# Optimization experiments

Hardware: AMD Instinct MI355X
Metric: run time of the kernel (lower is better)

The kernel has to match this reference:

```python
import jax, jax.numpy as jnp
import numpy as np

N_LINKS = 262144
N_PAIRS = 4194304
F = 20   # feature_size
R = 20   # readout_units
T = 4    # message passing iterations


def setup_inputs() -> dict:
    key = jax.random.key(0)
    ks = jax.random.split(key, 16)
    s = 0.1
    return {
        "link_state": jax.random.normal(ks[0], (N_LINKS, F), dtype=jnp.float32),
        "first": jax.random.randint(ks[1], (N_PAIRS,), 0, N_LINKS),
        "second": jax.random.randint(ks[2], (N_PAIRS,), 0, N_LINKS),
        "state_dim": F,
        # message MLP: Linear(2F -> F)
        "W_msg": jax.random.normal(ks[3], (F, 2 * F), dtype=jnp.float32) * s,
        "b_msg": jnp.zeros((F,), dtype=jnp.float32),
        # GRUCell params (PyTorch layout: [3F, in] with r,z,n gate order)
        "W_ih": jax.random.normal(ks[4], (3 * F, F), dtype=jnp.float32) * s,
        "W_hh": jax.random.normal(ks[5], (3 * F, F), dtype=jnp.float32) * s,
        "b_ih": jnp.zeros((3 * F,), dtype=jnp.float32),
        "b_hh": jnp.zeros((3 * F,), dtype=jnp.float32),
        # readout: Linear(F->R) SELU, Linear(R->R) SELU
        "W_r1": jax.random.normal(ks[6], (R, F), dtype=jnp.float32) * s,
        "b_r1": jnp.zeros((R,), dtype=jnp.float32),
        "W_r2": jax.random.normal(ks[7], (R, R), dtype=jnp.float32) * s,
        "b_r2": jnp.zeros((R,), dtype=jnp.float32),
        # out layer: Linear(R->1)
        "W_out": jax.random.normal(ks[8], (1, R), dtype=jnp.float32) * s,
        "b_out": jnp.zeros((1,), dtype=jnp.float32),
    }


def _gru_cell(m, h, W_ih, W_hh, b_ih, b_hh):
    # PyTorch GRUCell math, gate order (r, z, n)
    gi = m @ W_ih.T + b_ih   # [N, 3F]
    gh = h @ W_hh.T + b_hh   # [N, 3F]
    i_r, i_z, i_n = jnp.split(gi, 3, axis=1)
    h_r, h_z, h_n = jnp.split(gh, 3, axis=1)
    r = jax.nn.sigmoid(i_r + h_r)
    z = jax.nn.sigmoid(i_z + h_z)
    n = jnp.tanh(i_n + r * h_n)
    return (1.0 - z) * n + z * h


def reference(link_state, first, second, state_dim,
              W_msg, b_msg, W_ih, W_hh, b_ih, b_hh,
              W_r1, b_r1, W_r2, b_r2, W_out, b_out):
    state = link_state  # [N_LINKS, F]
    for _ in range(T):
        main_edges = state[first]    # gather [N_PAIRS, F]
        neigh_edges = state[second]  # gather [N_PAIRS, F]
        edges_concat = jnp.concatenate([main_edges, neigh_edges], axis=1)
        m = jax.nn.selu(edges_concat @ W_msg.T + b_msg)  # [N_PAIRS, F]
        agg = jnp.zeros_like(state).at[second].add(m)    # scatter_add back to links
        state = _gru_cell(agg, state, W_ih, W_hh, b_ih, b_hh)
    feature = jnp.sum(state, axis=0)  # [F]
    h1 = jax.nn.selu(W_r1 @ feature + b_r1)
    h2 = jax.nn.selu(W_r2 @ h1 + b_r2)
    return W_out @ h2 + b_out  # [1]
```

## Files before the change

### kernel.cpp

```cpp
#include <hip/hip_runtime.h>
#include <hip/hip_fp16.h>

#define N_LINKS 262144
#define N_PAIRS 4194304
#define F 20
#define XB 20
#define T_ITERS 4

#define NSB 256
#define LPS 1024
#define PB 256
#define PT 1024
#define PCHUNK (N_PAIRS / PB)
#define PPT (PCHUNK / PT)

typedef float f32x2 __attribute__((ext_vector_type(2)));
typedef _Float16 h16x2 __attribute__((ext_vector_type(2)));

__device__ __forceinline__ float selu_f(float x) {
    const float scale = 1.0507009873554805f;
    const float scale_alpha = 1.7580993408473766f;
    return x > 0.0f ? scale * x : scale_alpha * (__expf(x) - 1.0f);
}

__device__ __forceinline__ float selu_b(float x) {
    const float s = 1.0507009873554805f;
    const float sa = 1.7580993408473766f;
    const float mx = fmaxf(x, 0.0f);
    const float mn = fminf(x, 0.0f);
    return fmaf(sa, __expf(mn), fmaf(s, mx, -sa));
}

__device__ __forceinline__ float sigmoid_f(float x) {
    return 1.0f / (1.0f + __expf(-x));
}

__device__ __forceinline__ float tanh_fast(float x) {
    x = fminf(fmaxf(x, -15.0f), 15.0f);
    float e = __expf(2.0f * x);
    return (e - 1.0f) / (e + 1.0f);
}

__device__ __forceinline__ void store_row_fp8(unsigned char* rowp, const float* o1) {
    int* p = (int*)rowp;
#pragma unroll
    for (int i = 0; i < 5; ++i) {
        int w = 0;
        w = __builtin_amdgcn_cvt_pk_fp8_f32(o1[4*i+0], o1[4*i+1], w, false);
        w = __builtin_amdgcn_cvt_pk_fp8_f32(o1[4*i+2], o1[4*i+3], w, true);
        p[i] = w;
    }
}


__global__ void __launch_bounds__(PT)
k_part(const int* __restrict__ first, const int* __restrict__ second,
       int* __restrict__ ent, int* __restrict__ ptable, int* __restrict__ sectot) {
    __shared__ int hist[NSB];
    __shared__ int cur[NSB];
    const int b = blockIdx.x;
    const int cbase = b * PCHUNK;
    const int tid = threadIdx.x;
    for (int i = tid; i < NSB; i += PT) hist[i] = 0;
    __syncthreads();
    int sv[PPT];
#pragma unroll
    for (int k = 0; k < PPT; ++k) {
        sv[k] = second[cbase + k * PT + tid];
        atomicAdd(&hist[sv[k] >> 10], 1);
    }
    __syncthreads();
    if (tid < NSB) {
        int acc = 0;
        for (int j = 0; j < tid; ++j) acc += hist[j];
        cur[tid] = acc;
        ptable[b * (NSB + 1) + tid] = acc;
        if (tid == 0) ptable[b * (NSB + 1) + NSB] = PCHUNK;
        atomicAdd(&sectot[tid], hist[tid]);
    }
    __syncthreads();
#pragma unroll
    for (int k = 0; k < PPT; ++k) {
        const int s = sv[k];
        const int f = first[cbase + k * PT + tid];
        const int pos = atomicAdd(&cur[s >> 10], 1);
        ent[cbase + pos] = f | ((s & 1023) << 18);
    }
}

__global__ void k_scan256(const int* __restrict__ sectot, int* __restrict__ sbase,
                          int* __restrict__ rs) {
    __shared__ int s[NSB];
    const int t = threadIdx.x;
    s[t] = sectot[t];
    __syncthreads();
    if (t == 0) {
        int acc = 0;
        for (int j = 0; j < NSB; ++j) { int c = s[j]; s[j] = acc; acc += c; }
    }
    __syncthreads();
    sbase[t] = s[t];
    if (t == 0) { sbase[NSB] = N_PAIRS; rs[N_LINKS] = N_PAIRS; }
}

__global__ void __launch_bounds__(PT)
k_build(const int* __restrict__ ptable, const int* __restrict__ sbase,
        const int* __restrict__ ent, int* __restrict__ srcs, int* __restrict__ rs,
        int* __restrict__ lid) {
    __shared__ int rstart[PB];
    __shared__ int rlen[PB];
    __shared__ int lcnt[LPS];
    __shared__ int cur[LPS];
    __shared__ int dhist[64];
    __shared__ int dbase[64];
    __shared__ int dcur[64];
    const int sb = blockIdx.x;
    const int tid = threadIdx.x;
    if (tid < PB) {
        const int o0 = ptable[tid * (NSB + 1) + sb];
        const int o1 = ptable[tid * (NSB + 1) + sb + 1];
        rstart[tid] = tid * PCHUNK + o0;
        rlen[tid] = o1 - o0;
    }
    lcnt[tid] = 0;
    if (tid < 64) { dhist[tid] = 0; dcur[tid] = 0; }
    __syncthreads();
    const int wave = tid >> 6;
    const int lane = tid & 63;
    for (int j = wave; j < PB; j += (PT >> 6)) {
        const int r0 = rstart[j], rl = rlen[j];
        for (int i = lane; i < rl; i += 64)
            atomicAdd(&lcnt[(ent[r0 + i] >> 18) & 1023], 1);
    }
    __syncthreads();
    const int count = lcnt[tid];
    const int dbin = min(count, 63);
    atomicAdd(&dhist[dbin], 1);
    __syncthreads();
    if (tid == 0) {
        int acc = 0;
        for (int b = 0; b < 64; ++b) { dbase[b] = acc; acc += dhist[b]; }
    }
    __syncthreads();
    const int rank = dbase[dbin] + atomicAdd(&dcur[dbin], 1);
    lcnt[rank] = count;
    lid[sb * LPS + rank] = sb * LPS + tid;
    __syncthreads();
    for (int off = 1; off < LPS; off <<= 1) {
        const int v = (tid >= off) ? lcnt[tid - off] : 0;
        __syncthreads();
        lcnt[tid] += v;
        __syncthreads();
    }
    const int sbb = sbase[sb];
    const int excl = lcnt[rank] - count;
    rs[sb * LPS + rank] = sbb + excl;
    cur[tid] = excl;
    __syncthreads();
    for (int j = wave; j < PB; j += (PT >> 6)) {
        const int r0 = rstart[j], rl = rlen[j];
        for (int i = lane; i < rl; i += 64) {
            const int e = ent[r0 + i];
            const int pos = atomicAdd(&cur[(e >> 18) & 1023], 1);
            srcs[sbb + pos] = e & 0x3FFFF;
        }
    }
}

__global__ void k_inv(const int* __restrict__ lid, int* __restrict__ rnk) {
    const int i = blockIdx.x * blockDim.x + threadIdx.x;
    rnk[lid[i]] = i;
}

__global__ void k_remap(int* __restrict__ srcs, const int* __restrict__ rnk) {
    const int p = blockIdx.x * blockDim.x + threadIdx.x;
    srcs[p] = rnk[srcs[p]] * 20;
}


__global__ void k_premsg(const float* __restrict__ link_state,
                         const int* __restrict__ lid,
                         const float* __restrict__ W_msg,
                         const float* __restrict__ b_msg,
                         unsigned char* __restrict__ X1b, __half* __restrict__ X2h,
                         float* __restrict__ state_r) {
    __shared__ float Wl[F * 2 * F];
    __shared__ float bl[F];
    for (int i = threadIdx.x; i < F * 2 * F; i += blockDim.x) Wl[i] = W_msg[i];
    if (threadIdx.x < F) bl[threadIdx.x] = b_msg[threadIdx.x];
    __syncthreads();

    const int slot = blockIdx.x * blockDim.x + threadIdx.x;
    const int link = lid[slot];

    float s[F];
    const float4* sp = (const float4*)(link_state + (size_t)link * F);
    float4* so = (float4*)(state_r + (size_t)slot * F);
#pragma unroll
    for (int i = 0; i < 5; ++i) {
        float4 v = sp[i];
        so[i] = v;
        s[4*i+0] = v.x; s[4*i+1] = v.y; s[4*i+2] = v.z; s[4*i+3] = v.w;
    }
    float o1[F], o2[F];
#pragma unroll
    for (int o = 0; o < F; ++o) {
        float a1 = bl[o], a2 = 0.0f;
#pragma unroll
        for (int k = 0; k < F; ++k) {
            a1 = fmaf(Wl[o * 2 * F + k],     s[k], a1);
            a2 = fmaf(Wl[o * 2 * F + F + k], s[k], a2);
        }
        o1[o] = a1; o2[o] = a2;
    }
    store_row_fp8(X1b + (size_t)slot * XB, o1);
    __half2* xp = (__half2*)(X2h + (size_t)slot * F);
#pragma unroll
    for (int i = 0; i < 10; ++i)
        xp[i] = __halves2half2(__float2half(o2[2*i]), __float2half(o2[2*i+1]));
}

__global__ void __launch_bounds__(256)
k_agg(const int* __restrict__ rs, const int* __restrict__ srcs,
      const unsigned char* __restrict__ X1b, const __half* __restrict__ X2h,
      float* __restrict__ agg) {
    const int wave = threadIdx.x >> 6;
    const int lane = threadIdx.x & 63;
    const int g = lane / 10;
    const int j = lane - g * 10;
    const int gsel = (g < 6) ? g : 5;
    const int slot = (blockIdx.x * 4 + wave) * 6 + gsel;

    const bool active = (g < 6) && (slot < N_LINKS);
    const int sc = min(slot, N_LINKS - 1);
    const int row_start = rs[sc];
    const int cnt = active ? (rs[sc + 1] - row_start) : 0;
    const int cl = (cnt > 0) ? (cnt - 1) : 0;

    const __half2 hv = *(const __half2*)(X2h + (size_t)sc * F + 2 * j);
    const float x2a = __half2float(__low2half(hv));
    const float x2b = __half2float(__high2half(hv));

    int cmax = cnt;
#pragma unroll
    for (int off = 1; off < 64; off <<= 1)
        cmax = max(cmax, __shfl_xor(cmax, off, 64));

    float acc_a = 0.0f, acc_b = 0.0f;

    for (int base = 0; base < cmax; base += 10) {
        const int sv = srcs[row_start + min(base + j, cl)];
#pragma unroll
        for (int r = 0; r < 10; ++r) {
            const int src = __shfl(sv, gsel * 10 + r, 64);
            const unsigned v = *(const unsigned short*)(X1b + src + 2 * j);
            const f32x2 xx = __builtin_amdgcn_cvt_pk_f32_fp8((int)v, false);
            const bool ok = (base + r) < cnt;
            acc_a += ok ? selu_b(xx[0] + x2a) : 0.0f;
            acc_b += ok ? selu_b(xx[1] + x2b) : 0.0f;
        }
    }
    if (active) {
        float2 o; o.x = acc_a; o.y = acc_b;
        *(float2*)(agg + (size_t)slot * F + 2 * j) = o;
    }
}

__global__ void __launch_bounds__(256)
k_gru(const float* __restrict__ agg, const float* __restrict__ h_in,
      const float* __restrict__ W_ih, const float* __restrict__ W_hh,
      const float* __restrict__ b_ih, const float* __restrict__ b_hh,
      const float* __restrict__ W_msg, const float* __restrict__ b_msg,
      float* __restrict__ h_out, unsigned char* __restrict__ X1b,
      __half* __restrict__ X2h, float* __restrict__ feature, int flags) {
    __shared__ h16x2 WiH[3 * F * 10];
    __shared__ h16x2 WhH[3 * F * 10];
    __shared__ h16x2 WmH[F * 20];
    __shared__ float bi[3 * F];
    __shared__ float bh[3 * F];
    __shared__ float bm[F];
    __shared__ float red[4 * F];
    {
        _Float16* wi = (_Float16*)WiH;
        _Float16* wh = (_Float16*)WhH;
        for (int i = threadIdx.x; i < 3 * F * F; i += blockDim.x) {
            wi[i] = (_Float16)W_ih[i];
            wh[i] = (_Float16)W_hh[i];
        }
        _Float16* wm = (_Float16*)WmH;
        for (int i = threadIdx.x; i < F * 2 * F; i += blockDim.x)
            wm[i] = (_Float16)W_msg[i];
    }
    if (threadIdx.x < 3 * F) {
        bi[threadIdx.x] = b_ih[threadIdx.x];
        bh[threadIdx.x] = b_hh[threadIdx.x];
    }
    if (threadIdx.x < F) bm[threadIdx.x] = b_msg[threadIdx.x];
    __syncthreads();

    const int l = blockIdx.x * blockDim.x + threadIdx.x;

    float m[F], h[F];
    const float4* mp = (const float4*)(agg  + (size_t)l * F);
    const float4* hp = (const float4*)(h_in + (size_t)l * F);
#pragma unroll
    for (int i = 0; i < 5; ++i) {
        float4 vm = mp[i], vh = hp[i];
        m[4*i+0] = vm.x; m[4*i+1] = vm.y; m[4*i+2] = vm.z; m[4*i+3] = vm.w;
        h[4*i+0] = vh.x; h[4*i+1] = vh.y; h[4*i+2] = vh.z; h[4*i+3] = vh.w;
    }
    h16x2 mh[10], hh[10];
#pragma unroll
    for (int i = 0; i < 10; ++i) {
        mh[i][0] = (_Float16)m[2*i]; mh[i][1] = (_Float16)m[2*i+1];
        hh[i][0] = (_Float16)h[2*i]; hh[i][1] = (_Float16)h[2*i+1];
    }

    float hn[F];
#pragma unroll
    for (int j = 0; j < F; ++j) {
        float gri = 0.f, gzi = 0.f, gin = bi[2*F + j];
        float grh = 0.f, gzh = 0.f, ghn = bh[2*F + j];
#pragma unroll
        for (int k = 0; k < 10; ++k) {
            gri = __builtin_amdgcn_fdot2(WiH[(0*F + j) * 10 + k], mh[k], gri, false);
            gzi = __builtin_amdgcn_fdot2(WiH[(1*F + j) * 10 + k], mh[k], gzi, false);
            gin = __builtin_amdgcn_fdot2(WiH[(2*F + j) * 10 + k], mh[k], gin, false);
            grh = __builtin_amdgcn_fdot2(WhH[(0*F + j) * 10 + k], hh[k], grh, false);
            gzh = __builtin_amdgcn_fdot2(WhH[(1*F + j) * 10 + k], hh[k], gzh, false);
            ghn = __builtin_amdgcn_fdot2(WhH[(2*F + j) * 10 + k], hh[k], ghn, false);
        }
        float r = sigmoid_f(bi[j] + bh[j] + gri + grh);
        float z = sigmoid_f(bi[F + j] + bh[F + j] + gzi + gzh);
        float n = tanh_fast(gin + r * ghn);
        hn[j] = (1.0f - z) * n + z * h[j];
    }

    float4* op = (float4*)(h_out + (size_t)l * F);
#pragma unroll
    for (int i = 0; i < 5; ++i)
        op[i] = make_float4(hn[4*i], hn[4*i+1], hn[4*i+2], hn[4*i+3]);

    if (flags & 1) {
        h16x2 hnh[10];
#pragma unroll
        for (int i = 0; i < 10; ++i) {
            hnh[i][0] = (_Float16)hn[2*i]; hnh[i][1] = (_Float16)hn[2*i+1];
        }
        float o1[F], o2[F];
#pragma unroll
        for (int o = 0; o < F; ++o) {
            float a1 = bm[o], a2 = 0.0f;
#pragma unroll
            for (int k = 0; k < 10; ++k) {
                a1 = __builtin_amdgcn_fdot2(WmH[o * 20 + k],      hnh[k], a1, false);
                a2 = __builtin_amdgcn_fdot2(WmH[o * 20 + 10 + k], hnh[k], a2, false);
            }
            o1[o] = a1; o2[o] = a2;
        }
        store_row_fp8(X1b + (size_t)l * XB, o1);
        __half2* xp = (__half2*)(X2h + (size_t)l * F);
#pragma unroll
        for (int i = 0; i < 10; ++i)
            xp[i] = __halves2half2(__float2half(o2[2*i]), __float2half(o2[2*i+1]));
    }

    if (flags & 2) {
#pragma unroll
        for (int off = 1; off < 64; off <<= 1) {
#pragma unroll
            for (int j = 0; j < F; ++j) hn[j] += __shfl_xor(hn[j], off, 64);
        }
        const int lane = threadIdx.x & 63;
        const int wave = threadIdx.x >> 6;
        if (lane == 0) {
#pragma unroll
            for (int j = 0; j < F; ++j) red[wave * F + j] = hn[j];
        }
        __syncthreads();
        if (threadIdx.x < F) {
            float s = red[threadIdx.x] + red[F + threadIdx.x] +
                      red[2 * F + threadIdx.x] + red[3 * F + threadIdx.x];
            atomicAdd(&feature[threadIdx.x], s);
        }
    }
}

__global__ void k_readout(const float* __restrict__ feature,
                          const float* __restrict__ W_r1, const float* __restrict__ b_r1,
                          const float* __restrict__ W_r2, const float* __restrict__ b_r2,
                          const float* __restrict__ W_out, const float* __restrict__ b_out,
                          float* __restrict__ out) {
    if (threadIdx.x != 0 || blockIdx.x != 0) return;
    float fv[F], h1[F], h2[F];
#pragma unroll
    for (int i = 0; i < F; ++i) fv[i] = feature[i];
#pragma unroll
    for (int o = 0; o < F; ++o) {
        float a = b_r1[o];
#pragma unroll
        for (int k = 0; k < F; ++k) a = fmaf(W_r1[o * F + k], fv[k], a);
        h1[o] = selu_f(a);
    }
#pragma unroll
    for (int o = 0; o < F; ++o) {
        float a = b_r2[o];
#pragma unroll
        for (int k = 0; k < F; ++k) a = fmaf(W_r2[o * F + k], h1[k], a);
        h2[o] = selu_f(a);
    }
    float a = b_out[0];
#pragma unroll
    for (int k = 0; k < F; ++k) a = fmaf(W_out[k], h2[k], a);
    out[0] = a;
}

extern "C" void kernel_launch(void* const* d_in, const int* in_sizes, int n_in,
                              void* d_out, int out_size, void* d_ws, size_t ws_size,
                              hipStream_t stream) {
    const float* link_state = (const float*)d_in[0];
    const int*   first      = (const int*)  d_in[1];
    const int*   second     = (const int*)  d_in[2];
    const float* W_msg = (const float*)d_in[4];
    const float* b_msg = (const float*)d_in[5];
    const float* W_ih  = (const float*)d_in[6];
    const float* W_hh  = (const float*)d_in[7];
    const float* b_ih  = (const float*)d_in[8];
    const float* b_hh  = (const float*)d_in[9];
    const float* W_r1  = (const float*)d_in[10];
    const float* b_r1  = (const float*)d_in[11];
    const float* W_r2  = (const float*)d_in[12];
    const float* b_r2  = (const float*)d_in[13];
    const float* W_out = (const float*)d_in[14];
    const float* b_out = (const float*)d_in[15];
    float* out = (float*)d_out;

    const size_t NF = (size_t)N_LINKS * F;
    float* state   = (float*)d_ws;
    float* agg     = state + NF;
    unsigned char* X1b = (unsigned char*)(agg + NF);
    __half* X2h    = (__half*)(X1b + (size_t)N_LINKS * XB + 64);
    int*    srcs   = (int*)(X2h + NF);
    int*    rs     = srcs + N_PAIRS;
    int*    lid    = rs + N_LINKS + 1;
    int*    rnk    = lid + N_LINKS;
    float* feature = (float*)(rnk + N_LINKS);
    int* ptable    = (int*)(feature + 32);
    int* sectot    = ptable + PB * (NSB + 1);
    int* sbase     = sectot + NSB;
    int* ent       = (int*)agg;

    hipMemsetAsync(sectot, 0, NSB * sizeof(int), stream);
    hipMemsetAsync(feature, 0, F * sizeof(float), stream);

    k_part<<<PB, PT, 0, stream>>>(first, second, ent, ptable, sectot);
    k_scan256<<<1, NSB, 0, stream>>>(sectot, sbase, rs);
    k_build<<<NSB, PT, 0, stream>>>(ptable, sbase, ent, srcs, rs, lid);
    k_inv<<<N_LINKS / 256, 256, 0, stream>>>(lid, rnk);
    k_remap<<<N_PAIRS / 256, 256, 0, stream>>>(srcs, rnk);

    k_premsg<<<N_LINKS / 256, 256, 0, stream>>>(link_state, lid, W_msg, b_msg,
                                                X1b, X2h, state);
    const int aggBlocks = (N_LINKS + 23) / 24;
    for (int t = 0; t < T_ITERS; ++t) {
        int flags = (t < T_ITERS - 1 ? 1 : 0) | (t == T_ITERS - 1 ? 2 : 0);
        k_agg<<<aggBlocks, 256, 0, stream>>>(rs, srcs, X1b, X2h, agg);
        k_gru<<<N_LINKS / 256, 256, 0, stream>>>(agg, state, W_ih, W_hh, b_ih, b_hh,
                                                 W_msg, b_msg, state, X1b, X2h,
                                                 feature, flags);
    }
    k_readout<<<1, 64, 0, stream>>>(feature, W_r1, b_r1, W_r2, b_r2, W_out, b_out, out);
}
```

Before: 601.3 us.

## Fuse aggregation and GRU into one step kernel with double-buffered fp8 messages

Merges the per-iteration aggregation and GRU kernels into a single k_step kernel. The GRU and next-message projection are computed cooperatively by 10 lanes per link, using shuffles to share the aggregated message and hidden state, so the agg buffer round trip through global memory goes away. The fp8 X1 table is double-buffered because other links still read the current buffer while it would otherwise be overwritten. The rank inverse is now written inside k_build, which drops the k_inv launch. In exchange, every step block (about 11k of them) reloads and converts the weights into shared memory, and the GRU maths is spread across lanes with extra shuffles.

```diff
diff --git a/kernel.cpp b/kernel.cpp
--- a/kernel.cpp
+++ b/kernel.cpp
@@ -106,7 +106,7 @@
 __global__ void __launch_bounds__(PT)
 k_build(const int* __restrict__ ptable, const int* __restrict__ sbase,
         const int* __restrict__ ent, int* __restrict__ srcs, int* __restrict__ rs,
-        int* __restrict__ lid) {
+        int* __restrict__ lid, int* __restrict__ rnk_g) {
     __shared__ int rstart[PB];
     __shared__ int rlen[PB];
     __shared__ int lcnt[LPS];
@@ -145,6 +145,7 @@
     const int rank = dbase[dbin] + atomicAdd(&dcur[dbin], 1);
     lcnt[rank] = count;
     lid[sb * LPS + rank] = sb * LPS + tid;
+    rnk_g[sb * LPS + tid] = sb * LPS + rank;
     __syncthreads();
     for (int off = 1; off < LPS; off <<= 1) {
         const int v = (tid >= off) ? lcnt[tid - off] : 0;
@@ -165,11 +166,6 @@
             srcs[sbb + pos] = e & 0x3FFFF;
         }
     }
-}
-
-__global__ void k_inv(const int* __restrict__ lid, int* __restrict__ rnk) {
-    const int i = blockIdx.x * blockDim.x + threadIdx.x;
-    rnk[lid[i]] = i;
 }
 
 __global__ void k_remap(int* __restrict__ srcs, const int* __restrict__ rnk) {
@@ -221,18 +217,50 @@
 }
 
 __global__ void __launch_bounds__(256)
-k_agg(const int* __restrict__ rs, const int* __restrict__ srcs,
-      const unsigned char* __restrict__ X1b, const __half* __restrict__ X2h,
-      float* __restrict__ agg) {
+k_step(const int* __restrict__ rs, const int* __restrict__ srcs,
+       const unsigned char* __restrict__ X1cur, unsigned char* __restrict__ X1nxt,
+       __half* __restrict__ X2h, float* __restrict__ state,
+       const float* __restrict__ W_ih, const float* __restrict__ W_hh,
+       const float* __restrict__ b_ih, const float* __restrict__ b_hh,
+       const float* __restrict__ W_msg, const float* __restrict__ b_msg,
+       float* __restrict__ feature, int flags) {
+    __shared__ h16x2 WiH[3 * F * 10];
+    __shared__ h16x2 WhH[3 * F * 10];
+    __shared__ h16x2 WmH[F * 20];
+    __shared__ float bi[3 * F];
+    __shared__ float bh[3 * F];
+    __shared__ float bm[F];
+    __shared__ float red[F];
+    {
+        _Float16* wi = (_Float16*)WiH;
+        _Float16* wh = (_Float16*)WhH;
+        for (int i = threadIdx.x; i < 3 * F * F; i += 256) {
+            wi[i] = (_Float16)W_ih[i];
+            wh[i] = (_Float16)W_hh[i];
+        }
+        _Float16* wm = (_Float16*)WmH;
+        for (int i = threadIdx.x; i < F * 2 * F; i += 256)
+            wm[i] = (_Float16)W_msg[i];
+    }
+    if (threadIdx.x < 3 * F) {
+        bi[threadIdx.x] = b_ih[threadIdx.x];
+        bh[threadIdx.x] = b_hh[threadIdx.x];
+    }
+    if (threadIdx.x < F) {
+        bm[threadIdx.x] = b_msg[threadIdx.x];
+        red[threadIdx.x] = 0.0f;
+    }
+    __syncthreads();
+
     const int wave = threadIdx.x >> 6;
     const int lane = threadIdx.x & 63;
     const int g = lane / 10;
     const int j = lane - g * 10;
     const int gsel = (g < 6) ? g : 5;
     const int slot = (blockIdx.x * 4 + wave) * 6 + gsel;
-
     const bool active = (g < 6) && (slot < N_LINKS);
     const int sc = min(slot, N_LINKS - 1);
+
     const int row_start = rs[sc];
     const int cnt = active ? (rs[sc + 1] - row_start) : 0;
     const int cl = (cnt > 0) ? (cnt - 1) : 0;
@@ -247,142 +275,93 @@
         cmax = max(cmax, __shfl_xor(cmax, off, 64));
 
     float acc_a = 0.0f, acc_b = 0.0f;
-
     for (int base = 0; base < cmax; base += 10) {
         const int sv = srcs[row_start + min(base + j, cl)];
 #pragma unroll
         for (int r = 0; r < 10; ++r) {
             const int src = __shfl(sv, gsel * 10 + r, 64);
-            const unsigned v = *(const unsigned short*)(X1b + src + 2 * j);
+            const unsigned v = *(const unsigned short*)(X1cur + src + 2 * j);
             const f32x2 xx = __builtin_amdgcn_cvt_pk_f32_fp8((int)v, false);
             const bool ok = (base + r) < cnt;
             acc_a += ok ? selu_b(xx[0] + x2a) : 0.0f;
             acc_b += ok ? selu_b(xx[1] + x2b) : 0.0f;
         }
     }
+
+    const float2 hown = *(const float2*)(state + (size_t)sc * F + 2 * j);
+    const int gb = gsel * 10;
+    h16x2 mh[10], hh[10];
+#pragma unroll
+    for (int kk = 0; kk < 10; ++kk) {
+        const float ma = __shfl(acc_a, gb + kk, 64);
+        const float mb = __shfl(acc_b, gb + kk, 64);
+        const float ha = __shfl(hown.x, gb + kk, 64);
+        const float hb = __shfl(hown.y, gb + kk, 64);
+        mh[kk][0] = (_Float16)ma; mh[kk][1] = (_Float16)mb;
+        hh[kk][0] = (_Float16)ha; hh[kk][1] = (_Float16)hb;
+    }
+
+    float hnv[2];
+    const float how[2] = {hown.x, hown.y};
+#pragma unroll
+    for (int t2 = 0; t2 < 2; ++t2) {
+        const int o = 2 * j + t2;
+        float gri = 0.f, gzi = 0.f, gin = bi[2*F + o];
+        float grh = 0.f, gzh = 0.f, ghn = bh[2*F + o];
+#pragma unroll
+        for (int kk = 0; kk < 10; ++kk) {
+            gri = __builtin_amdgcn_fdot2(WiH[(0*F + o) * 10 + kk], mh[kk], gri, false);
+            gzi = __builtin_amdgcn_fdot2(WiH[(1*F + o) * 10 + kk], mh[kk], gzi, false);
+            gin = __builtin_amdgcn_fdot2(WiH[(2*F + o) * 10 + kk], mh[kk], gin, false);
+            grh = __builtin_amdgcn_fdot2(WhH[(0*F + o) * 10 + kk], hh[kk], grh, false);
+            gzh = __builtin_amdgcn_fdot2(WhH[(1*F + o) * 10 + kk], hh[kk], gzh, false);
+            ghn = __builtin_amdgcn_fdot2(WhH[(2*F + o) * 10 + kk], hh[kk], ghn, false);
+        }
+        const float r = sigmoid_f(bi[o] + bh[o] + gri + grh);
+        const float z = sigmoid_f(bi[F + o] + bh[F + o] + gzi + gzh);
+        const float n = tanh_fast(gin + r * ghn);
+        hnv[t2] = (1.0f - z) * n + z * how[t2];
+    }
     if (active) {
-        float2 o; o.x = acc_a; o.y = acc_b;
-        *(float2*)(agg + (size_t)slot * F + 2 * j) = o;
-    }
-}
-
-__global__ void __launch_bounds__(256)
-k_gru(const float* __restrict__ agg, const float* __restrict__ h_in,
-      const float* __restrict__ W_ih, const float* __restrict__ W_hh,
-      const float* __restrict__ b_ih, const float* __restrict__ b_hh,
-      const float* __restrict__ W_msg, const float* __restrict__ b_msg,
-      float* __restrict__ h_out, unsigned char* __restrict__ X1b,
-      __half* __restrict__ X2h, float* __restrict__ feature, int flags) {
-    __shared__ h16x2 WiH[3 * F * 10];
-    __shared__ h16x2 WhH[3 * F * 10];
-    __shared__ h16x2 WmH[F * 20];
-    __shared__ float bi[3 * F];
-    __shared__ float bh[3 * F];
-    __shared__ float bm[F];
-    __shared__ float red[4 * F];
-    {
-        _Float16* wi = (_Float16*)WiH;
-        _Float16* wh = (_Float16*)WhH;
-        for (int i = threadIdx.x; i < 3 * F * F; i += blockDim.x) {
-            wi[i] = (_Float16)W_ih[i];
-            wh[i] = (_Float16)W_hh[i];
-        }
-        _Float16* wm = (_Float16*)WmH;
-        for (int i = threadIdx.x; i < F * 2 * F; i += blockDim.x)
-            wm[i] = (_Float16)W_msg[i];
-    }
-    if (threadIdx.x < 3 * F) {
-        bi[threadIdx.x] = b_ih[threadIdx.x];
-        bh[threadIdx.x] = b_hh[threadIdx.x];
-    }
-    if (threadIdx.x < F) bm[threadIdx.x] = b_msg[threadIdx.x];
-    __syncthreads();
-
-    const int l = blockIdx.x * blockDim.x + threadIdx.x;
-
-    float m[F], h[F];
-    const float4* mp = (const float4*)(agg  + (size_t)l * F);
-    const float4* hp = (const float4*)(h_in + (size_t)l * F);
-#pragma unroll
-    for (int i = 0; i < 5; ++i) {
-        float4 vm = mp[i], vh = hp[i];
-        m[4*i+0] = vm.x; m[4*i+1] = vm.y; m[4*i+2] = vm.z; m[4*i+3] = vm.w;
-        h[4*i+0] = vh.x; h[4*i+1] = vh.y; h[4*i+2] = vh.z; h[4*i+3] = vh.w;
-    }
-    h16x2 mh[10], hh[10];
-#pragma unroll
-    for (int i = 0; i < 10; ++i) {
-        mh[i][0] = (_Float16)m[2*i]; mh[i][1] = (_Float16)m[2*i+1];
-        hh[i][0] = (_Float16)h[2*i]; hh[i][1] = (_Float16)h[2*i+1];
-    }
-
-    float hn[F];
-#pragma unroll
-    for (int j = 0; j < F; ++j) {
-        float gri = 0.f, gzi = 0.f, gin = bi[2*F + j];
-        float grh = 0.f, gzh = 0.f, ghn = bh[2*F + j];
-#pragma unroll
-        for (int k = 0; k < 10; ++k) {
-            gri = __builtin_amdgcn_fdot2(WiH[(0*F + j) * 10 + k], mh[k], gri, false);
-            gzi = __builtin_amdgcn_fdot2(WiH[(1*F + j) * 10 + k], mh[k], gzi, false);
-            gin = __builtin_amdgcn_fdot2(WiH[(2*F + j) * 10 + k], mh[k], gin, false);
-            grh = __builtin_amdgcn_fdot2(WhH[(0*F + j) * 10 + k], hh[k], grh, false);
-            gzh = __builtin_amdgcn_fdot2(WhH[(1*F + j) * 10 + k], hh[k], gzh, false);
-            ghn = __builtin_amdgcn_fdot2(WhH[(2*F + j) * 10 + k], hh[k], ghn, false);
-        }
-        float r = sigmoid_f(bi[j] + bh[j] + gri + grh);
-        float z = sigmoid_f(bi[F + j] + bh[F + j] + gzi + gzh);
-        float n = tanh_fast(gin + r * ghn);
-        hn[j] = (1.0f - z) * n + z * h[j];
-    }
-
-    float4* op = (float4*)(h_out + (size_t)l * F);
-#pragma unroll
-    for (int i = 0; i < 5; ++i)
-        op[i] = make_float4(hn[4*i], hn[4*i+1], hn[4*i+2], hn[4*i+3]);
+        float2 o; o.x = hnv[0]; o.y = hnv[1];
+        *(float2*)(state + (size_t)slot * F + 2 * j) = o;
+    }
 
     if (flags & 1) {
         h16x2 hnh[10];
 #pragma unroll
-        for (int i = 0; i < 10; ++i) {
-            hnh[i][0] = (_Float16)hn[2*i]; hnh[i][1] = (_Float16)hn[2*i+1];
-        }
-        float o1[F], o2[F];
-#pragma unroll
-        for (int o = 0; o < F; ++o) {
+        for (int kk = 0; kk < 10; ++kk) {
+            const float na = __shfl(hnv[0], gb + kk, 64);
+            const float nb = __shfl(hnv[1], gb + kk, 64);
+            hnh[kk][0] = (_Float16)na; hnh[kk][1] = (_Float16)nb;
+        }
+        float o1v[2], o2v[2];
+#pragma unroll
+        for (int t2 = 0; t2 < 2; ++t2) {
+            const int o = 2 * j + t2;
             float a1 = bm[o], a2 = 0.0f;
 #pragma unroll
-            for (int k = 0; k < 10; ++k) {
-                a1 = __builtin_amdgcn_fdot2(WmH[o * 20 + k],      hnh[k], a1, false);
-                a2 = __builtin_amdgcn_fdot2(WmH[o * 20 + 10 + k], hnh[k], a2, false);
+            for (int kk = 0; kk < 10; ++kk) {
+                a1 = __builtin_amdgcn_fdot2(WmH[o * 20 + kk],      hnh[kk], a1, false);
+                a2 = __builtin_amdgcn_fdot2(WmH[o * 20 + 10 + kk], hnh[kk], a2, false);
             }
-            o1[o] = a1; o2[o] = a2;
-        }
-        store_row_fp8(X1b + (size_t)l * XB, o1);
-        __half2* xp = (__half2*)(X2h + (size_t)l * F);
-#pragma unroll
-        for (int i = 0; i < 10; ++i)
-            xp[i] = __halves2half2(__float2half(o2[2*i]), __float2half(o2[2*i+1]));
+            o1v[t2] = a1; o2v[t2] = a2;
+        }
+        if (active) {
+            const int w = __builtin_amdgcn_cvt_pk_fp8_f32(o1v[0], o1v[1], 0, false);
+            *(unsigned short*)(X1nxt + (size_t)slot * XB + 2 * j) = (unsigned short)w;
+            *(__half2*)(X2h + (size_t)slot * F + 2 * j) =
+                __halves2half2(__float2half(o2v[0]), __float2half(o2v[1]));
+        }
     }
 
     if (flags & 2) {
-#pragma unroll
-        for (int off = 1; off < 64; off <<= 1) {
-#pragma unroll
-            for (int j = 0; j < F; ++j) hn[j] += __shfl_xor(hn[j], off, 64);
-        }
-        const int lane = threadIdx.x & 63;
-        const int wave = threadIdx.x >> 6;
-        if (lane == 0) {
-#pragma unroll
-            for (int j = 0; j < F; ++j) red[wave * F + j] = hn[j];
+        if (active) {
+            atomicAdd(&red[2 * j],     hnv[0]);
+            atomicAdd(&red[2 * j + 1], hnv[1]);
         }
         __syncthreads();
-        if (threadIdx.x < F) {
-            float s = red[threadIdx.x] + red[F + threadIdx.x] +
-                      red[2 * F + threadIdx.x] + red[3 * F + threadIdx.x];
-            atomicAdd(&feature[threadIdx.x], s);
-        }
+        if (threadIdx.x < F) atomicAdd(&feature[threadIdx.x], red[threadIdx.x]);
     }
 }
 
@@ -436,38 +415,38 @@
     float* out = (float*)d_out;
 
     const size_t NF = (size_t)N_LINKS * F;
-    float* state   = (float*)d_ws;
-    float* agg     = state + NF;
-    unsigned char* X1b = (unsigned char*)(agg + NF);
-    __half* X2h    = (__half*)(X1b + (size_t)N_LINKS * XB + 64);
-    int*    srcs   = (int*)(X2h + NF);
-    int*    rs     = srcs + N_PAIRS;
-    int*    lid    = rs + N_LINKS + 1;
-    int*    rnk    = lid + N_LINKS;
+    float* state = (float*)d_ws;
+    unsigned char* X1b0 = (unsigned char*)(state + NF);
+    unsigned char* X1b1 = X1b0 + (size_t)N_LINKS * XB;
+    __half* X2h = (__half*)(X1b1 + (size_t)N_LINKS * XB);
+    int* srcs   = (int*)(X2h + NF);
+    int* rs     = srcs + N_PAIRS;
+    int* lid    = rs + N_LINKS + 1;
+    int* rnk    = lid + N_LINKS;
     float* feature = (float*)(rnk + N_LINKS);
-    int* ptable    = (int*)(feature + 32);
-    int* sectot    = ptable + PB * (NSB + 1);
-    int* sbase     = sectot + NSB;
-    int* ent       = (int*)agg;
+    int* ptable = (int*)(feature + 32);
+    int* sectot = ptable + PB * (NSB + 1);
+    int* sbase  = sectot + NSB;
+    int* ent    = (int*)X1b0;
 
     hipMemsetAsync(sectot, 0, NSB * sizeof(int), stream);
     hipMemsetAsync(feature, 0, F * sizeof(float), stream);
 
     k_part<<<PB, PT, 0, stream>>>(first, second, ent, ptable, sectot);
     k_scan256<<<1, NSB, 0, stream>>>(sectot, sbase, rs);
-    k_build<<<NSB, PT, 0, stream>>>(ptable, sbase, ent, srcs, rs, lid);
-    k_inv<<<N_LINKS / 256, 256, 0, stream>>>(lid, rnk);
+    k_build<<<NSB, PT, 0, stream>>>(ptable, sbase, ent, srcs, rs, lid, rnk);
     k_remap<<<N_PAIRS / 256, 256, 0, stream>>>(srcs, rnk);
 
     k_premsg<<<N_LINKS / 256, 256, 0, stream>>>(link_state, lid, W_msg, b_msg,
-                                                X1b, X2h, state);
-    const int aggBlocks = (N_LINKS + 23) / 24;
+                                                X1b0, X2h, state);
+
+    unsigned char* bufs[2] = {X1b0, X1b1};
+    const int stepBlocks = (N_LINKS + 23) / 24;
     for (int t = 0; t < T_ITERS; ++t) {
         int flags = (t < T_ITERS - 1 ? 1 : 0) | (t == T_ITERS - 1 ? 2 : 0);
-        k_agg<<<aggBlocks, 256, 0, stream>>>(rs, srcs, X1b, X2h, agg);
-        k_gru<<<N_LINKS / 256, 256, 0, stream>>>(agg, state, W_ih, W_hh, b_ih, b_hh,
-                                                 W_msg, b_msg, state, X1b, X2h,
-                                                 feature, flags);
+        k_step<<<stepBlocks, 256, 0, stream>>>(rs, srcs, bufs[t & 1], bufs[(t + 1) & 1],
+                                               X2h, state, W_ih, W_hh, b_ih, b_hh,
+                                               W_msg, b_msg, feature, flags);
     }
     k_readout<<<1, 64, 0, stream>>>(feature, W_r1, b_r1, W_r2, b_r2, W_out, b_out, out);
 }
```

Result: slower. 673.2 us (+12.0%).

## Process two links per GRU thread and fold rank inversion into build

Applied to the files above, without the earlier changes.

The GRU kernel now handles two links per thread. It loads each weight row from LDS into registers once and reuses it for both links, halving the grid size. The separate inverse-permutation kernel is removed, and k_build writes the rank table directly. This cuts LDS weight reads and one launch, but raises register pressure, which may reduce occupancy for the GRU kernel.

```diff
diff --git a/kernel.cpp b/kernel.cpp
--- a/kernel.cpp
+++ b/kernel.cpp
@@ -106,7 +106,7 @@
 __global__ void __launch_bounds__(PT)
 k_build(const int* __restrict__ ptable, const int* __restrict__ sbase,
         const int* __restrict__ ent, int* __restrict__ srcs, int* __restrict__ rs,
-        int* __restrict__ lid) {
+        int* __restrict__ lid, int* __restrict__ rnk_g) {
     __shared__ int rstart[PB];
     __shared__ int rlen[PB];
     __shared__ int lcnt[LPS];
@@ -145,6 +145,7 @@
     const int rank = dbase[dbin] + atomicAdd(&dcur[dbin], 1);
     lcnt[rank] = count;
     lid[sb * LPS + rank] = sb * LPS + tid;
+    rnk_g[sb * LPS + tid] = sb * LPS + rank;
     __syncthreads();
     for (int off = 1; off < LPS; off <<= 1) {
         const int v = (tid >= off) ? lcnt[tid - off] : 0;
@@ -165,11 +166,6 @@
             srcs[sbb + pos] = e & 0x3FFFF;
         }
     }
-}
-
-__global__ void k_inv(const int* __restrict__ lid, int* __restrict__ rnk) {
-    const int i = blockIdx.x * blockDim.x + threadIdx.x;
-    rnk[lid[i]] = i;
 }
 
 __global__ void k_remap(int* __restrict__ srcs, const int* __restrict__ rnk) {
@@ -267,12 +263,12 @@
 }
 
 __global__ void __launch_bounds__(256)
-k_gru(const float* __restrict__ agg, const float* __restrict__ h_in,
+k_gru(const float* __restrict__ agg, float* __restrict__ state,
       const float* __restrict__ W_ih, const float* __restrict__ W_hh,
       const float* __restrict__ b_ih, const float* __restrict__ b_hh,
       const float* __restrict__ W_msg, const float* __restrict__ b_msg,
-      float* __restrict__ h_out, unsigned char* __restrict__ X1b,
-      __half* __restrict__ X2h, float* __restrict__ feature, int flags) {
+      unsigned char* __restrict__ X1b, __half* __restrict__ X2h,
+      float* __restrict__ feature, int flags) {
     __shared__ h16x2 WiH[3 * F * 10];
     __shared__ h16x2 WhH[3 * F * 10];
     __shared__ h16x2 WmH[F * 20];
@@ -283,12 +279,12 @@
     {
         _Float16* wi = (_Float16*)WiH;
         _Float16* wh = (_Float16*)WhH;
-        for (int i = threadIdx.x; i < 3 * F * F; i += blockDim.x) {
+        for (int i = threadIdx.x; i < 3 * F * F; i += 256) {
             wi[i] = (_Float16)W_ih[i];
             wh[i] = (_Float16)W_hh[i];
         }
         _Float16* wm = (_Float16*)WmH;
-        for (int i = threadIdx.x; i < F * 2 * F; i += blockDim.x)
+        for (int i = threadIdx.x; i < F * 2 * F; i += 256)
             wm[i] = (_Float16)W_msg[i];
     }
     if (threadIdx.x < 3 * F) {
@@ -298,84 +294,146 @@
     if (threadIdx.x < F) bm[threadIdx.x] = b_msg[threadIdx.x];
     __syncthreads();
 
-    const int l = blockIdx.x * blockDim.x + threadIdx.x;
-
-    float m[F], h[F];
-    const float4* mp = (const float4*)(agg  + (size_t)l * F);
-    const float4* hp = (const float4*)(h_in + (size_t)l * F);
-#pragma unroll
-    for (int i = 0; i < 5; ++i) {
-        float4 vm = mp[i], vh = hp[i];
-        m[4*i+0] = vm.x; m[4*i+1] = vm.y; m[4*i+2] = vm.z; m[4*i+3] = vm.w;
-        h[4*i+0] = vh.x; h[4*i+1] = vh.y; h[4*i+2] = vh.z; h[4*i+3] = vh.w;
-    }
-    h16x2 mh[10], hh[10];
-#pragma unroll
-    for (int i = 0; i < 10; ++i) {
-        mh[i][0] = (_Float16)m[2*i]; mh[i][1] = (_Float16)m[2*i+1];
-        hh[i][0] = (_Float16)h[2*i]; hh[i][1] = (_Float16)h[2*i+1];
-    }
-
-    float hn[F];
-#pragma unroll
-    for (int j = 0; j < F; ++j) {
-        float gri = 0.f, gzi = 0.f, gin = bi[2*F + j];
-        float grh = 0.f, gzh = 0.f, ghn = bh[2*F + j];
-#pragma unroll
-        for (int k = 0; k < 10; ++k) {
-            gri = __builtin_amdgcn_fdot2(WiH[(0*F + j) * 10 + k], mh[k], gri, false);
-            gzi = __builtin_amdgcn_fdot2(WiH[(1*F + j) * 10 + k], mh[k], gzi, false);
-            gin = __builtin_amdgcn_fdot2(WiH[(2*F + j) * 10 + k], mh[k], gin, false);
-            grh = __builtin_amdgcn_fdot2(WhH[(0*F + j) * 10 + k], hh[k], grh, false);
-            gzh = __builtin_amdgcn_fdot2(WhH[(1*F + j) * 10 + k], hh[k], gzh, false);
-            ghn = __builtin_amdgcn_fdot2(WhH[(2*F + j) * 10 + k], hh[k], ghn, false);
-        }
-        float r = sigmoid_f(bi[j] + bh[j] + gri + grh);
-        float z = sigmoid_f(bi[F + j] + bh[F + j] + gzi + gzh);
-        float n = tanh_fast(gin + r * ghn);
-        hn[j] = (1.0f - z) * n + z * h[j];
-    }
-
-    float4* op = (float4*)(h_out + (size_t)l * F);
-#pragma unroll
-    for (int i = 0; i < 5; ++i)
-        op[i] = make_float4(hn[4*i], hn[4*i+1], hn[4*i+2], hn[4*i+3]);
+    const int l0 = (blockIdx.x * blockDim.x + threadIdx.x) * 2;
+
+    h16x2 mh[2][10], hh[2][10];
+#pragma unroll
+    for (int L = 0; L < 2; ++L) {
+        const float4* mp = (const float4*)(agg   + (size_t)(l0 + L) * F);
+        const float4* hp = (const float4*)(state + (size_t)(l0 + L) * F);
+#pragma unroll
+        for (int i = 0; i < 5; ++i) {
+            const float4 vm = mp[i], vh = hp[i];
+            mh[L][2*i+0][0] = (_Float16)vm.x; mh[L][2*i+0][1] = (_Float16)vm.y;
+            mh[L][2*i+1][0] = (_Float16)vm.z; mh[L][2*i+1][1] = (_Float16)vm.w;
+            hh[L][2*i+0][0] = (_Float16)vh.x; hh[L][2*i+0][1] = (_Float16)vh.y;
+            hh[L][2*i+1][0] = (_Float16)vh.z; hh[L][2*i+1][1] = (_Float16)vh.w;
+        }
+    }
+
+    float hn[2][F];
+#pragma unroll
+    for (int o = 0; o < F; ++o) {
+        float sr[2], sz[2], sni[2], snh[2];
+        {
+            h16x2 wi[10], wh[10];
+#pragma unroll
+            for (int kk = 0; kk < 10; ++kk) {
+                wi[kk] = WiH[(0*F + o) * 10 + kk];
+                wh[kk] = WhH[(0*F + o) * 10 + kk];
+            }
+#pragma unroll
+            for (int L = 0; L < 2; ++L) {
+                float a = bi[o] + bh[o];
+#pragma unroll
+                for (int kk = 0; kk < 10; ++kk) {
+                    a = __builtin_amdgcn_fdot2(wi[kk], mh[L][kk], a, false);
+                    a = __builtin_amdgcn_fdot2(wh[kk], hh[L][kk], a, false);
+                }
+                sr[L] = a;
+            }
+        }
+        {
+            h16x2 wi[10], wh[10];
+#pragma unroll
+            for (int kk = 0; kk < 10; ++kk) {
+                wi[kk] = WiH[(1*F + o) * 10 + kk];
+                wh[kk] = WhH[(1*F + o) * 10 + kk];
+            }
+#pragma unroll
+            for (int L = 0; L < 2; ++L) {
+                float a = bi[F + o] + bh[F + o];
+#pragma unroll
+                for (int kk = 0; kk < 10; ++kk) {
+                    a = __builtin_amdgcn_fdot2(wi[kk], mh[L][kk], a, false);
+                    a = __builtin_amdgcn_fdot2(wh[kk], hh[L][kk], a, false);
+                }
+                sz[L] = a;
+            }
+        }
+        {
+            h16x2 wi[10], wh[10];
+#pragma unroll
+            for (int kk = 0; kk < 10; ++kk) {
+                wi[kk] = WiH[(2*F + o) * 10 + kk];
+                wh[kk] = WhH[(2*F + o) * 10 + kk];
+            }
+#pragma unroll
+            for (int L = 0; L < 2; ++L) {
+                float ai = bi[2*F + o], ah = bh[2*F + o];
+#pragma unroll
+                for (int kk = 0; kk < 10; ++kk) {
+                    ai = __builtin_amdgcn_fdot2(wi[kk], mh[L][kk], ai, false);
+                    ah = __builtin_amdgcn_fdot2(wh[kk], hh[L][kk], ah, false);
+                }
+                sni[L] = ai; snh[L] = ah;
+            }
+        }
+#pragma unroll
+        for (int L = 0; L < 2; ++L) {
+            const float r = sigmoid_f(sr[L]);
+            const float z = sigmoid_f(sz[L]);
+            const float n = tanh_fast(sni[L] + r * snh[L]);
+            const float hO = (float)hh[L][o >> 1][o & 1];
+            hn[L][o] = (1.0f - z) * n + z * hO;
+        }
+    }
+
+#pragma unroll
+    for (int L = 0; L < 2; ++L) {
+        float4* op = (float4*)(state + (size_t)(l0 + L) * F);
+#pragma unroll
+        for (int i = 0; i < 5; ++i)
+            op[i] = make_float4(hn[L][4*i], hn[L][4*i+1], hn[L][4*i+2], hn[L][4*i+3]);
+    }
 
     if (flags & 1) {
-        h16x2 hnh[10];
-#pragma unroll
-        for (int i = 0; i < 10; ++i) {
-            hnh[i][0] = (_Float16)hn[2*i]; hnh[i][1] = (_Float16)hn[2*i+1];
-        }
-        float o1[F], o2[F];
-#pragma unroll
-        for (int o = 0; o < F; ++o) {
-            float a1 = bm[o], a2 = 0.0f;
-#pragma unroll
-            for (int k = 0; k < 10; ++k) {
-                a1 = __builtin_amdgcn_fdot2(WmH[o * 20 + k],      hnh[k], a1, false);
-                a2 = __builtin_amdgcn_fdot2(WmH[o * 20 + 10 + k], hnh[k], a2, false);
-            }
-            o1[o] = a1; o2[o] = a2;
-        }
-        store_row_fp8(X1b + (size_t)l * XB, o1);
-        __half2* xp = (__half2*)(X2h + (size_t)l * F);
-#pragma unroll
-        for (int i = 0; i < 10; ++i)
-            xp[i] = __halves2half2(__float2half(o2[2*i]), __float2half(o2[2*i+1]));
+#pragma unroll
+        for (int L = 0; L < 2; ++L) {
+            h16x2 hnh[10];
+#pragma unroll
+            for (int i = 0; i < 10; ++i) {
+                hnh[i][0] = (_Float16)hn[L][2*i]; hnh[i][1] = (_Float16)hn[L][2*i+1];
+            }
+            float o1[F], o2[F];
+#pragma unroll
+            for (int o = 0; o < F; ++o) {
+                h16x2 w1[10], w2[10];
+#pragma unroll
+                for (int kk = 0; kk < 10; ++kk) {
+                    w1[kk] = WmH[o * 20 + kk];
+                    w2[kk] = WmH[o * 20 + 10 + kk];
+                }
+                float a1 = bm[o], a2 = 0.0f;
+#pragma unroll
+                for (int kk = 0; kk < 10; ++kk) {
+                    a1 = __builtin_amdgcn_fdot2(w1[kk], hnh[kk], a1, false);
+                    a2 = __builtin_amdgcn_fdot2(w2[kk], hnh[kk], a2, false);
+                }
+                o1[o] = a1; o2[o] = a2;
+            }
+            store_row_fp8(X1b + (size_t)(l0 + L) * XB, o1);
+            __half2* xp = (__half2*)(X2h + (size_t)(l0 + L) * F);
+#pragma unroll
+            for (int i = 0; i < 10; ++i)
+                xp[i] = __halves2half2(__float2half(o2[2*i]), __float2half(o2[2*i+1]));
+        }
     }
 
     if (flags & 2) {
+        float hs[F];
+#pragma unroll
+        for (int jj = 0; jj < F; ++jj) hs[jj] = hn[0][jj] + hn[1][jj];
 #pragma unroll
         for (int off = 1; off < 64; off <<= 1) {
 #pragma unroll
-            for (int j = 0; j < F; ++j) hn[j] += __shfl_xor(hn[j], off, 64);
+            for (int jj = 0; jj < F; ++jj) hs[jj] += __shfl_xor(hs[jj], off, 64);
         }
         const int lane = threadIdx.x & 63;
         const int wave = threadIdx.x >> 6;
         if (lane == 0) {
 #pragma unroll
-            for (int j = 0; j < F; ++j) red[wave * F + j] = hn[j];
+            for (int jj = 0; jj < F; ++jj) red[wave * F + jj] = hs[jj];
         }
         __syncthreads();
         if (threadIdx.x < F) {
@@ -436,37 +494,37 @@
     float* out = (float*)d_out;
 
     const size_t NF = (size_t)N_LINKS * F;
-    float* state   = (float*)d_ws;
-    float* agg     = state + NF;
+    float* state = (float*)d_ws;
+    float* agg   = state + NF;
     unsigned char* X1b = (unsigned char*)(agg + NF);
-    __half* X2h    = (__half*)(X1b + (size_t)N_LINKS * XB + 64);
-    int*    srcs   = (int*)(X2h + NF);
-    int*    rs     = srcs + N_PAIRS;
-    int*    lid    = rs + N_LINKS + 1;
-    int*    rnk    = lid + N_LINKS;
+    __half* X2h = (__half*)(X1b + (size_t)N_LINKS * XB + 64);
+    int* srcs   = (int*)(X2h + NF);
+    int* rs     = srcs + N_PAIRS;
+    int* lid    = rs + N_LINKS + 1;
+    int* rnk    = lid + N_LINKS;
     float* feature = (float*)(rnk + N_LINKS);
-    int* ptable    = (int*)(feature + 32);
-    int* sectot    = ptable + PB * (NSB + 1);
-    int* sbase     = sectot + NSB;
-    int* ent       = (int*)agg;
+    int* ptable = (int*)(feature + 32);
+    int* sectot = ptable + PB * (NSB + 1);
+    int* sbase  = sectot + NSB;
+    int* ent    = (int*)agg;
 
     hipMemsetAsync(sectot, 0, NSB * sizeof(int), stream);
     hipMemsetAsync(feature, 0, F * sizeof(float), stream);
 
     k_part<<<PB, PT, 0, stream>>>(first, second, ent, ptable, sectot);
     k_scan256<<<1, NSB, 0, stream>>>(sectot, sbase, rs);
-    k_build<<<NSB, PT, 0, stream>>>(ptable, sbase, ent, srcs, rs, lid);
-    k_inv<<<N_LINKS / 256, 256, 0, stream>>>(lid, rnk);
+    k_build<<<NSB, PT, 0, stream>>>(ptable, sbase, ent, srcs, rs, lid, rnk);
     k_remap<<<N_PAIRS / 256, 256, 0, stream>>>(srcs, rnk);
 
     k_premsg<<<N_LINKS / 256, 256, 0, stream>>>(link_state, lid, W_msg, b_msg,
                                                 X1b, X2h, state);
+
     const int aggBlocks = (N_LINKS + 23) / 24;
     for (int t = 0; t < T_ITERS; ++t) {
         int flags = (t < T_ITERS - 1 ? 1 : 0) | (t == T_ITERS - 1 ? 2 : 0);
         k_agg<<<aggBlocks, 256, 0, stream>>>(rs, srcs, X1b, X2h, agg);
-        k_gru<<<N_LINKS / 256, 256, 0, stream>>>(agg, state, W_ih, W_hh, b_ih, b_hh,
-                                                 W_msg, b_msg, state, X1b, X2h,
+        k_gru<<<N_LINKS / 512, 256, 0, stream>>>(agg, state, W_ih, W_hh, b_ih, b_hh,
+                                                 W_msg, b_msg, X1b, X2h,
                                                  feature, flags);
     }
     k_readout<<<1, 64, 0, stream>>>(feature, W_r1, b_r1, W_r2, b_r2, W_out, b_out, out);
```

Result: slower. 749.6 us (+24.7%).
